# Performance work log

Measured on AMD Instinct MI355X. Metric: run time of the kernel, lower is better.

## Reference

```python
import jax, jax.numpy as jnp
import numpy as np

N_AGENTS = 8
N_ACTIONS = 16
SAMPLE = 16
STATE_DIM = 256
EMBED = 256
IN_DIM = N_AGENTS * N_ACTIONS + STATE_DIM  # 384


def setup_inputs() -> dict:
    key = jax.random.key(0)
    ks = jax.random.split(key, 12)
    bs, t = 32, 32
    s = 0.05
    return {
        "states": jax.random.normal(ks[0], (bs, t, STATE_DIM), jnp.float32),
        "agent_qs": jax.random.normal(ks[1], (bs, t, N_AGENTS, N_ACTIONS), jnp.float32),
        "W1": jax.random.normal(ks[2], (IN_DIM, EMBED), jnp.float32) * s,
        "b1": jnp.zeros((EMBED,), jnp.float32),
        "W2": jax.random.normal(ks[3], (EMBED, EMBED), jnp.float32) * s,
        "b2": jnp.zeros((EMBED,), jnp.float32),
        "W3": jax.random.normal(ks[4], (EMBED, 1), jnp.float32) * s,
        "b3": jnp.zeros((1,), jnp.float32),
        "Vw1": jax.random.normal(ks[5], (STATE_DIM, EMBED), jnp.float32) * s,
        "Vb1": jnp.zeros((EMBED,), jnp.float32),
        "Vw2": jax.random.normal(ks[6], (EMBED, 1), jnp.float32) * s,
        "Vb2": jnp.zeros((1,), jnp.float32),
    }


def reference(states, agent_qs, W1, b1, W2, b2, W3, b3, Vw1, Vb1, Vw2, Vb2):
    bs, t = states.shape[0], states.shape[1]
    B = bs * t
    A, NA, S, sd = N_AGENTS, N_ACTIONS, SAMPLE, STATE_DIM
    st = states.reshape(B, sd)
    qs = agent_qs.reshape(B, A, NA)

    # --- sample grand coalitions (random permutation per (B,S) row) ---
    perm_key = jax.random.key(42)
    u = jax.random.uniform(perm_key, (B, S, A))
    pos = jnp.argsort(u, axis=-1)          # grand_coalitions_pos: agent i -> position pos[i]
    inv = jnp.argsort(pos, axis=-1)        # grand_coalitions: position j -> agent inv[j]

    indiv = jax.nn.one_hot(pos, A, dtype=st.dtype)                         # (B,S,A,A)
    subcoal = (jnp.arange(A)[None, None, None, :] <= pos[..., None]).astype(st.dtype)
    no_i = subcoal - indiv                                                 # coalition members excl. self

    # reorder agent qs along position dim: reordered[b,s,j,:] = qs[b, inv[b,s,j], :]
    reordered = jnp.take_along_axis(
        jnp.broadcast_to(qs[:, None], (B, S, A, NA)), inv[..., None], axis=2)

    # (B,S,A,A,NA): detach contribution of other coalition members
    coal = (jax.lax.stop_gradient(reordered[:, :, None] * no_i[..., None])
            + reordered[:, :, None] * indiv[..., None])

    x = coal.reshape(B * S * A, A * NA)
    stx = jnp.broadcast_to(st[:, None, None], (B, S, A, sd)).reshape(B * S * A, sd)
    inp = jnp.concatenate([stx, x], axis=1)

    h = jax.nn.relu(inp @ W1 + b1)
    h = jax.nn.relu(h @ W2 + b2)
    advs = h @ W3 + b3
    v = jax.nn.relu(stx @ Vw1 + Vb1) @ Vw2 + Vb2

    marginal = (advs + v).reshape(B, S, A)
    shapley = marginal.mean(axis=1)        # mean over samples
    return shapley.reshape(bs, t, A)
```

## Files before the change

### kernel.cpp

```cpp
#include <hip/hip_runtime.h>


#define A_N   8
#define NA_N  16
#define S_N   16
#define SD    256
#define EMB   256
#define B_TOT 1024

typedef __bf16 bf16x8 __attribute__((ext_vector_type(8)));
typedef float  f32x4  __attribute__((ext_vector_type(4)));

__device__ __forceinline__ f32x4 splat4(float v) {
  f32x4 x; x[0] = v; x[1] = v; x[2] = v; x[3] = v; return x;
}
__device__ __forceinline__ bf16x8 zero8() {
  bf16x8 z;
#pragma unroll
  for (int j = 0; j < 8; ++j) z[j] = (__bf16)0.0f;
  return z;
}

__device__ __forceinline__ float jax_uniform(unsigned idx) {
  const unsigned ks0 = 0u, ks1 = 42u, ks2 = 0x1BD11BDAu ^ 42u;
  unsigned x0 = 0u + ks0;
  unsigned x1 = idx + ks1;
#define TF_RND(r) { x0 += x1; x1 = (x1 << (r)) | (x1 >> (32 - (r))); x1 ^= x0; }
  TF_RND(13) TF_RND(15) TF_RND(26) TF_RND(6)  x0 += ks1; x1 += ks2 + 1u;
  TF_RND(17) TF_RND(29) TF_RND(16) TF_RND(24) x0 += ks2; x1 += ks0 + 2u;
  TF_RND(13) TF_RND(15) TF_RND(26) TF_RND(6)  x0 += ks0; x1 += ks1 + 3u;
  TF_RND(17) TF_RND(29) TF_RND(16) TF_RND(24) x0 += ks1; x1 += ks2 + 4u;
  TF_RND(13) TF_RND(15) TF_RND(26) TF_RND(6)  x0 += ks2; x1 += ks0 + 5u;
#undef TF_RND
  const unsigned bits = x0 ^ x1;
  return __uint_as_float((bits >> 9) | 0x3F800000u) - 1.0f;
}

__global__ __launch_bounds__(256) void prep_kernel(
    const float* __restrict__ states, const float* __restrict__ W1,
    const float* __restrict__ b1, const float* __restrict__ Vw1,
    const float* __restrict__ Vb1, const float* __restrict__ Vw2,
    const float* __restrict__ Vb2, float* __restrict__ sW,
    float* __restrict__ vout) {
  __shared__ float st_l[2][SD];
  __shared__ float red_l[2][4];
  const int b0 = blockIdx.x * 2;
  const int n = threadIdx.x;

#pragma unroll
  for (int i = 0; i < 2; ++i) st_l[i][n] = states[(b0 + i) * SD + n];
  __syncthreads();

  float aS[2], aV[2];
  const float b1n = b1[n], vb1n = Vb1[n];
#pragma unroll
  for (int i = 0; i < 2; ++i) { aS[i] = b1n; aV[i] = vb1n; }

#pragma unroll 8
  for (int k = 0; k < SD; ++k) {
    const float wv = W1[k * EMB + n];
    const float vw = Vw1[k * EMB + n];
#pragma unroll
    for (int i = 0; i < 2; ++i) {
      const float s = st_l[i][k];
      aS[i] = fmaf(s, wv, aS[i]);
      aV[i] = fmaf(s, vw, aV[i]);
    }
  }
#pragma unroll
  for (int i = 0; i < 2; ++i) sW[(b0 + i) * EMB + n] = aS[i];

  const float vw2 = Vw2[n];
#pragma unroll
  for (int i = 0; i < 2; ++i) {
    float c = fmaxf(aV[i], 0.f) * vw2;
#pragma unroll
    for (int off = 32; off; off >>= 1) c += __shfl_down(c, off);
    if ((n & 63) == 0) red_l[i][n >> 6] = c;
  }
  __syncthreads();
  if (n < 2)
    vout[b0 + n] = red_l[n][0] + red_l[n][1] + red_l[n][2] + red_l[n][3] + Vb2[0];
}

__global__ __launch_bounds__(256) void pack_kernel(
    const float* __restrict__ W1, const float* __restrict__ W2,
    __bf16* __restrict__ W1b_bf, __bf16* __restrict__ W2_bf) {
  const int ts = blockIdx.x * 256 + threadIdx.x;
  if (ts < 4096) {
    const int t = ts >> 10, rem = ts & 1023, u = rem >> 6, L = rem & 63;
    const int q = L >> 4, l15 = L & 15;
#pragma unroll
    for (int j = 0; j < 8; ++j) {
      const int k = t * 32 + q * 8 + j, nn = u * 16 + l15;
      W1b_bf[ts * 8 + j] = (__bf16)W1[(SD + k) * EMB + nn];
    }
  } else {
    const int ts2 = ts - 4096;
    const int t = ts2 >> 10, rem = ts2 & 1023, u = rem >> 6, L = rem & 63;
    const int q = L >> 4, l15 = L & 15;
#pragma unroll
    for (int j = 0; j < 8; ++j) {
      const int k = t * 32 + q * 8 + j, nn = u * 16 + l15;
      W2_bf[ts2 * 8 + j] = (__bf16)W2[k * EMB + nn];
    }
  }
}

__global__ __launch_bounds__(256, 4) void main_kernel(
    const float* __restrict__ agent_qs, const float* __restrict__ b2g,
    const float* __restrict__ W3, const float* __restrict__ b3,
    const float* __restrict__ sW, const float* __restrict__ vv,
    const __bf16* __restrict__ W1b_bf, const __bf16* __restrict__ W2_bf,
    float* __restrict__ out) {
  __shared__ bf16x8 h1_l[32 * 64];
  __shared__ __attribute__((aligned(16))) __bf16 qs_bf[A_N * NA_N];
  __shared__ float u_l[128];
  __shared__ int   inv_l[128];
  __shared__ int   pos_l[128];
  __shared__ float adv_part[4][64];
  __shared__ float marg_l[128];

  const int b = blockIdx.x;
  const int n = threadIdx.x;
  const int w = n >> 6, L = n & 63, q = L >> 4, l15 = L & 15;

  if (n < 128) {
    qs_bf[n] = (__bf16)agent_qs[b * 128 + n];
    u_l[n] = jax_uniform((unsigned)(b * 128 + n));
  }
  __syncthreads();

  if (n < 128) {
    const int s = n >> 3, a = n & 7;
    const float u = u_l[n];
    int r = 0;
#pragma unroll
    for (int a2 = 0; a2 < A_N; ++a2) {
      const float u2 = u_l[s * 8 + a2];
      r += (u2 < u || (u2 == u && a2 < a)) ? 1 : 0;
    }
    inv_l[n] = r;
    pos_l[s * 8 + r] = a;
  }
  __syncthreads();

  const int i_pref  = l15 & 7;
  const int sl_half = l15 >> 3;
  const int jq      = q >> 1;
  const int na0     = (q & 1) * 8;

  for (int p = 0; p < 2; ++p) {
#pragma unroll 1
    for (int nh = 0; nh < 2; ++nh) {
      f32x4 acc[4][2];
#pragma unroll
      for (int i = 0; i < 2; ++i) {
        const float sv = sW[b * EMB + (w * 4 + nh * 2 + i) * 16 + l15];
#pragma unroll
        for (int mt = 0; mt < 4; ++mt) acc[mt][i] = splat4(sv);
      }
#pragma unroll 2
      for (int t = 0; t < 4; ++t) {
        const int jcoal = t * 2 + jq;
        const bool on = (jcoal <= i_pref);
        bf16x8 bfr[2];
#pragma unroll
        for (int i = 0; i < 2; ++i)
          bfr[i] = *(const bf16x8*)
              &W1b_bf[((t * 16 + w * 4 + nh * 2 + i) * 64 + L) * 8];
#pragma unroll
        for (int mt = 0; mt < 4; ++mt) {
          const int ag = inv_l[(p * 8 + mt * 2 + sl_half) * 8 + jcoal];
          const bf16x8 qv = *(const bf16x8*)&qs_bf[ag * NA_N + na0];
          const bf16x8 af = on ? qv : zero8();
#pragma unroll
          for (int i = 0; i < 2; ++i)
            acc[mt][i] = __builtin_amdgcn_mfma_f32_16x16x32_bf16(
                af, bfr[i], acc[mt][i], 0, 0, 0);
        }
      }
      __bf16* h1e = (__bf16*)h1_l;
#pragma unroll
      for (int i = 0; i < 2; ++i) {
        const int c = (w * 4 + nh * 2 + i) * 16 + l15;
        const int t2 = c >> 5, q2 = (c >> 3) & 3, j2 = l15 & 7;
#pragma unroll
        for (int mt = 0; mt < 4; ++mt) {
#pragma unroll
          for (int r = 0; r < 4; ++r) {
            const float v = fmaxf(acc[mt][i][r], 0.f);
            h1e[(((t2 * 4 + mt) * 64) + q2 * 16 + q * 4 + r) * 8 + j2] =
                (__bf16)v;
          }
        }
      }
    }
    __syncthreads();

    float psum[4][4];
#pragma unroll
    for (int mt = 0; mt < 4; ++mt)
#pragma unroll
      for (int r = 0; r < 4; ++r) psum[mt][r] = 0.f;

#pragma unroll 1
    for (int nh = 0; nh < 2; ++nh) {
      f32x4 acc[4][2];
#pragma unroll
      for (int i = 0; i < 2; ++i) {
        const float bv = b2g[(w * 4 + nh * 2 + i) * 16 + l15];
#pragma unroll
        for (int mt = 0; mt < 4; ++mt) acc[mt][i] = splat4(bv);
      }
#pragma unroll 2
      for (int t = 0; t < 8; ++t) {
        bf16x8 bfr[2];
#pragma unroll
        for (int i = 0; i < 2; ++i)
          bfr[i] = *(const bf16x8*)
              &W2_bf[((t * 16 + w * 4 + nh * 2 + i) * 64 + L) * 8];
#pragma unroll
        for (int mt = 0; mt < 4; ++mt) {
          const bf16x8 af = h1_l[(t * 4 + mt) * 64 + L];
#pragma unroll
          for (int i = 0; i < 2; ++i)
            acc[mt][i] = __builtin_amdgcn_mfma_f32_16x16x32_bf16(
                af, bfr[i], acc[mt][i], 0, 0, 0);
        }
      }
#pragma unroll
      for (int i = 0; i < 2; ++i) {
        const float w3v = W3[(w * 4 + nh * 2 + i) * 16 + l15];
#pragma unroll
        for (int mt = 0; mt < 4; ++mt)
#pragma unroll
          for (int r = 0; r < 4; ++r)
            psum[mt][r] = fmaf(fmaxf(acc[mt][i][r], 0.f), w3v, psum[mt][r]);
      }
    }

#pragma unroll
    for (int mt = 0; mt < 4; ++mt) {
#pragma unroll
      for (int r = 0; r < 4; ++r) {
        float sum = psum[mt][r];
#pragma unroll
        for (int off = 1; off < 16; off <<= 1) sum += __shfl_xor(sum, off);
        if (l15 == 0) adv_part[w][mt * 16 + q * 4 + r] = sum;
      }
    }
    __syncthreads();
    if (n < 64)
      marg_l[p * 64 + n] = adv_part[0][n] + adv_part[1][n] +
                           adv_part[2][n] + adv_part[3][n];
    __syncthreads();
  }

  if (n < A_N) {
    float sh = 0.f;
#pragma unroll
    for (int s = 0; s < S_N; ++s) sh += marg_l[s * 8 + pos_l[s * 8 + n]];
    out[b * A_N + n] = sh * (1.f / 16.f) + b3[0] + vv[b];
  }
}

extern "C" void kernel_launch(void* const* d_in, const int* in_sizes, int n_in,
                              void* d_out, int out_size, void* d_ws,
                              size_t ws_size, hipStream_t stream) {
  const float* states   = (const float*)d_in[0];
  const float* agent_qs = (const float*)d_in[1];
  const float* W1       = (const float*)d_in[2];
  const float* b1       = (const float*)d_in[3];
  const float* W2       = (const float*)d_in[4];
  const float* b2       = (const float*)d_in[5];
  const float* W3       = (const float*)d_in[6];
  const float* b3       = (const float*)d_in[7];
  const float* Vw1      = (const float*)d_in[8];
  const float* Vb1      = (const float*)d_in[9];
  const float* Vw2      = (const float*)d_in[10];
  const float* Vb2      = (const float*)d_in[11];
  float* out = (float*)d_out;

  char* ws = (char*)d_ws;
  float*  sW     = (float*)(ws);
  float*  vv     = (float*)(ws + 1048576);
  __bf16* W1b_bf = (__bf16*)(ws + 1052672);
  __bf16* W2_bf  = (__bf16*)(ws + 1118208);

  prep_kernel<<<512, 256, 0, stream>>>(states, W1, b1, Vw1, Vb1, Vw2, Vb2,
                                       sW, vv);
  pack_kernel<<<48, 256, 0, stream>>>(W1, W2, W1b_bf, W2_bf);
  main_kernel<<<B_TOT, 256, 0, stream>>>(agent_qs, b2, W3, b3, sW, vv,
                                         W1b_bf, W2_bf, out);
}
```

Measured before the change: 122.6 us.

## Replace scalar state-projection prep kernel with bf16 MFMA GEMM

Drops the scalar FMA prep kernel that computed states@W1[:256] and the value-network hidden layer. In its place, W1's state rows and Vw1 are packed into one bf16 MFMA-tiled matrix and a 64-block MFMA GEMM computes both, with the value head reduced through atomicAdd into a zero-initialised buffer. The goal is to cut the time of the fp32 prep stage. In exchange it adds a memset, bf16 rounding of states and weights in this projection, and atomic accumulation order nondeterminism.

```diff
diff --git a/kernel.cpp b/kernel.cpp
--- a/kernel.cpp
+++ b/kernel.cpp
@@ -36,56 +36,10 @@
   return __uint_as_float((bits >> 9) | 0x3F800000u) - 1.0f;
 }
 
-__global__ __launch_bounds__(256) void prep_kernel(
-    const float* __restrict__ states, const float* __restrict__ W1,
-    const float* __restrict__ b1, const float* __restrict__ Vw1,
-    const float* __restrict__ Vb1, const float* __restrict__ Vw2,
-    const float* __restrict__ Vb2, float* __restrict__ sW,
-    float* __restrict__ vout) {
-  __shared__ float st_l[2][SD];
-  __shared__ float red_l[2][4];
-  const int b0 = blockIdx.x * 2;
-  const int n = threadIdx.x;
-
-#pragma unroll
-  for (int i = 0; i < 2; ++i) st_l[i][n] = states[(b0 + i) * SD + n];
-  __syncthreads();
-
-  float aS[2], aV[2];
-  const float b1n = b1[n], vb1n = Vb1[n];
-#pragma unroll
-  for (int i = 0; i < 2; ++i) { aS[i] = b1n; aV[i] = vb1n; }
-
-#pragma unroll 8
-  for (int k = 0; k < SD; ++k) {
-    const float wv = W1[k * EMB + n];
-    const float vw = Vw1[k * EMB + n];
-#pragma unroll
-    for (int i = 0; i < 2; ++i) {
-      const float s = st_l[i][k];
-      aS[i] = fmaf(s, wv, aS[i]);
-      aV[i] = fmaf(s, vw, aV[i]);
-    }
-  }
-#pragma unroll
-  for (int i = 0; i < 2; ++i) sW[(b0 + i) * EMB + n] = aS[i];
-
-  const float vw2 = Vw2[n];
-#pragma unroll
-  for (int i = 0; i < 2; ++i) {
-    float c = fmaxf(aV[i], 0.f) * vw2;
-#pragma unroll
-    for (int off = 32; off; off >>= 1) c += __shfl_down(c, off);
-    if ((n & 63) == 0) red_l[i][n >> 6] = c;
-  }
-  __syncthreads();
-  if (n < 2)
-    vout[b0 + n] = red_l[n][0] + red_l[n][1] + red_l[n][2] + red_l[n][3] + Vb2[0];
-}
-
 __global__ __launch_bounds__(256) void pack_kernel(
     const float* __restrict__ W1, const float* __restrict__ W2,
-    __bf16* __restrict__ W1b_bf, __bf16* __restrict__ W2_bf) {
+    const float* __restrict__ Vw1, __bf16* __restrict__ W1b_bf,
+    __bf16* __restrict__ W2_bf, __bf16* __restrict__ PW_bf) {
   const int ts = blockIdx.x * 256 + threadIdx.x;
   if (ts < 4096) {
     const int t = ts >> 10, rem = ts & 1023, u = rem >> 6, L = rem & 63;
@@ -95,7 +49,7 @@
       const int k = t * 32 + q * 8 + j, nn = u * 16 + l15;
       W1b_bf[ts * 8 + j] = (__bf16)W1[(SD + k) * EMB + nn];
     }
-  } else {
+  } else if (ts < 12288) {
     const int ts2 = ts - 4096;
     const int t = ts2 >> 10, rem = ts2 & 1023, u = rem >> 6, L = rem & 63;
     const int q = L >> 4, l15 = L & 15;
@@ -104,15 +58,96 @@
       const int k = t * 32 + q * 8 + j, nn = u * 16 + l15;
       W2_bf[ts2 * 8 + j] = (__bf16)W2[k * EMB + nn];
     }
+  } else {
+    const int ts3 = ts - 12288;
+    const int t = ts3 >> 11, rem = ts3 & 2047, u = rem >> 6, L = rem & 63;
+    const int q = L >> 4, l15 = L & 15;
+#pragma unroll
+    for (int j = 0; j < 8; ++j) {
+      const int k = t * 32 + q * 8 + j, nn = u * 16 + l15;
+      const float v = (nn < EMB) ? W1[k * EMB + nn]
+                                 : Vw1[k * EMB + (nn - EMB)];
+      PW_bf[ts3 * 8 + j] = (__bf16)v;
+    }
+  }
+}
+
+__global__ __launch_bounds__(256) void prep_mfma_kernel(
+    const float* __restrict__ states, const float* __restrict__ b1,
+    const float* __restrict__ Vb1, const float* __restrict__ Vw2,
+    const __bf16* __restrict__ PW_bf, float* __restrict__ sW,
+    float* __restrict__ vv) {
+  const int mi = blockIdx.x >> 2;
+  const int ni = blockIdx.x & 3;
+  const int n = threadIdx.x;
+  const int w = n >> 6, L = n & 63, q = L >> 4, l15 = L & 15;
+
+  f32x4 acc[4][2];
+#pragma unroll
+  for (int ui = 0; ui < 2; ++ui) {
+    const int col = (ni * 8 + w * 2 + ui) * 16 + l15;
+    const float bias = (col < EMB) ? b1[col] : Vb1[col - EMB];
+#pragma unroll
+    for (int mt = 0; mt < 4; ++mt) acc[mt][ui] = splat4(bias);
+  }
+
+#pragma unroll 2
+  for (int t = 0; t < 8; ++t) {
+    bf16x8 bfr[2];
+#pragma unroll
+    for (int ui = 0; ui < 2; ++ui) {
+      const int u = ni * 8 + w * 2 + ui;
+      bfr[ui] = *(const bf16x8*)&PW_bf[((t * 32 + u) * 64 + L) * 8];
+    }
+#pragma unroll
+    for (int mt = 0; mt < 4; ++mt) {
+      const float* srow = &states[(mi * 64 + mt * 16 + l15) * SD + t * 32 + q * 8];
+      bf16x8 af;
+#pragma unroll
+      for (int j = 0; j < 8; ++j) af[j] = (__bf16)srow[j];
+#pragma unroll
+      for (int ui = 0; ui < 2; ++ui)
+        acc[mt][ui] = __builtin_amdgcn_mfma_f32_16x16x32_bf16(
+            af, bfr[ui], acc[mt][ui], 0, 0, 0);
+    }
+  }
+
+  if (ni < 2) {
+#pragma unroll
+    for (int ui = 0; ui < 2; ++ui) {
+      const int col = (ni * 8 + w * 2 + ui) * 16 + l15;
+#pragma unroll
+      for (int mt = 0; mt < 4; ++mt)
+#pragma unroll
+        for (int r = 0; r < 4; ++r)
+          sW[(mi * 64 + mt * 16 + q * 4 + r) * EMB + col] = acc[mt][ui][r];
+    }
+  } else {
+#pragma unroll
+    for (int mt = 0; mt < 4; ++mt) {
+#pragma unroll
+      for (int r = 0; r < 4; ++r) {
+        float p = 0.f;
+#pragma unroll
+        for (int ui = 0; ui < 2; ++ui) {
+          const int colV = (ni * 8 + w * 2 + ui) * 16 + l15 - EMB;
+          p = fmaf(fmaxf(acc[mt][ui][r], 0.f), Vw2[colV], p);
+        }
+#pragma unroll
+        for (int off = 1; off < 16; off <<= 1) p += __shfl_xor(p, off);
+        if (l15 == 0)
+          atomicAdd(&vv[mi * 64 + mt * 16 + q * 4 + r], p);
+      }
+    }
   }
 }
 
 __global__ __launch_bounds__(256, 4) void main_kernel(
     const float* __restrict__ agent_qs, const float* __restrict__ b2g,
     const float* __restrict__ W3, const float* __restrict__ b3,
-    const float* __restrict__ sW, const float* __restrict__ vv,
-    const __bf16* __restrict__ W1b_bf, const __bf16* __restrict__ W2_bf,
-    float* __restrict__ out) {
+    const float* __restrict__ Vb2, const float* __restrict__ sW,
+    const float* __restrict__ vv, const __bf16* __restrict__ W1b_bf,
+    const __bf16* __restrict__ W2_bf, float* __restrict__ out) {
   __shared__ bf16x8 h1_l[32 * 64];
   __shared__ __attribute__((aligned(16))) __bf16 qs_bf[A_N * NA_N];
   __shared__ float u_l[128];
@@ -261,7 +296,7 @@
     float sh = 0.f;
 #pragma unroll
     for (int s = 0; s < S_N; ++s) sh += marg_l[s * 8 + pos_l[s * 8 + n]];
-    out[b * A_N + n] = sh * (1.f / 16.f) + b3[0] + vv[b];
+    out[b * A_N + n] = sh * (1.f / 16.f) + b3[0] + Vb2[0] + vv[b];
   }
 }
 
@@ -287,10 +322,12 @@
   float*  vv     = (float*)(ws + 1048576);
   __bf16* W1b_bf = (__bf16*)(ws + 1052672);
   __bf16* W2_bf  = (__bf16*)(ws + 1118208);
-
-  prep_kernel<<<512, 256, 0, stream>>>(states, W1, b1, Vw1, Vb1, Vw2, Vb2,
-                                       sW, vv);
-  pack_kernel<<<48, 256, 0, stream>>>(W1, W2, W1b_bf, W2_bf);
-  main_kernel<<<B_TOT, 256, 0, stream>>>(agent_qs, b2, W3, b3, sW, vv,
+  __bf16* PW_bf  = (__bf16*)(ws + 1249280);
+
+  hipMemsetAsync(vv, 0, B_TOT * sizeof(float), stream);
+  pack_kernel<<<112, 256, 0, stream>>>(W1, W2, Vw1, W1b_bf, W2_bf, PW_bf);
+  prep_mfma_kernel<<<64, 256, 0, stream>>>(states, b1, Vb1, Vw2, PW_bf,
+                                           sW, vv);
+  main_kernel<<<B_TOT, 256, 0, stream>>>(agent_qs, b2, W3, b3, Vb2, sW, vv,
                                          W1b_bf, W2_bf, out);
 }
```

Result: no change. 124.9 us (+1.8%).
